# Kernel optimization log

Hardware: AMD Instinct MI355X
Metric: run time of the kernel (lower is better)

The kernel has to match this reference:

```python
import jax, jax.numpy as jnp
import numpy as np

N = 50000
E = 600000
D_IN = 128
D_HID = 128


def gcn_conv(x, src, dst, ew, W, b):
    """PyG-style GCNConv with self-loops and symmetric normalization.
    x: [N, Fin], src/dst: [E'], ew: [E'], W: [Fin, Fout], b: [Fout].
    """
    n = x.shape[0]
    # degree from incoming edge weights (self-loops already appended)
    deg = jax.ops.segment_sum(ew, dst, num_segments=n)
    dinv = jnp.where(deg > 0, jax.lax.rsqrt(deg), 0.0)
    norm = dinv[src] * ew * dinv[dst]  # [E']
    h = x @ W  # linear transform first (PyG order)
    msg = h[src] * norm[:, None]  # gather + scale, [E', Fout]
    out = jax.ops.segment_sum(msg, dst, num_segments=n)  # scatter-add
    return out + b


def setup_inputs() -> dict:
    key = jax.random.key(0)
    k1, k2, k3, k4, k5, k6, k7 = jax.random.split(key, 7)
    x = jax.random.normal(k1, (N, D_IN), dtype=jnp.float32)
    edge_index = jax.random.randint(k2, (2, E), 0, N, dtype=jnp.int64)
    edge_weight = jax.random.uniform(k3, (E,), dtype=jnp.float32)
    s1 = 1.0 / np.sqrt(D_IN)
    s2 = 1.0 / np.sqrt(D_HID)
    W1 = jax.random.uniform(k4, (D_IN, D_HID), dtype=jnp.float32, minval=-s1, maxval=s1)
    b1 = jax.random.uniform(k5, (D_HID,), dtype=jnp.float32, minval=-s1, maxval=s1)
    W2 = jax.random.uniform(k6, (D_HID, D_IN), dtype=jnp.float32, minval=-s2, maxval=s2)
    b2 = jax.random.uniform(k7, (D_IN,), dtype=jnp.float32, minval=-s2, maxval=s2)
    return {"x": x, "edge_index": edge_index, "edge_weight": edge_weight,
            "W1": W1, "b1": b1, "W2": W2, "b2": b2}


def reference(x, edge_index, edge_weight, W1, b1, W2, b2):
    n = x.shape[0]
    loops = jnp.arange(n, dtype=edge_index.dtype)
    src = jnp.concatenate([edge_index[0], loops])
    dst = jnp.concatenate([edge_index[1], loops])
    ew = jnp.concatenate([edge_weight, jnp.ones((n,), dtype=edge_weight.dtype)])
    h = gcn_conv(x, src, dst, ew, W1, b1)
    h = jax.nn.relu(h)
    h = gcn_conv(h, src, dst, ew, W2, b2)
    return jax.nn.sigmoid(h)
```

## Files before the change

kernel.cpp:

```cpp
#include <hip/hip_runtime.h>
#include <math.h>


typedef unsigned int uint32;
typedef unsigned long long u64;
typedef __attribute__((ext_vector_type(8))) short bf16x8;
typedef __attribute__((ext_vector_type(4))) float f32x4;
typedef __attribute__((ext_vector_type(2))) float f32x2;

__device__ __forceinline__ unsigned short f2bf(float f) {
    uint32 b = __float_as_uint(f);
    return (unsigned short)((b + 0x7FFFu + ((b >> 16) & 1u)) >> 16);
}

template <int AFP32, int OUTFP8>
__device__ __forceinline__ void gemm_body(const void* __restrict__ Ap,
                                          const unsigned short* __restrict__ WT,
                                          void* __restrict__ H,
                                          int n, int tb) {
    const int lane = threadIdx.x & 63;
    const int wv   = threadIdx.x >> 6;
    const int quad = lane >> 4;
    const int l16  = lane & 15;
    const int m0   = tb * 128 + wv * 32;
    f32x4 acc[2][8] = {};

    #pragma unroll
    for (int ks = 0; ks < 4; ++ks) {
        const int k0 = ks * 32 + quad * 8;
        bf16x8 a[2];
        #pragma unroll
        for (int rt = 0; rt < 2; ++rt) {
            int row = m0 + rt * 16 + l16;
            if (row >= n) row = n - 1;
            if (AFP32) {
                const float* Af = (const float*)Ap + (size_t)row * 128 + k0;
                float4 f0 = *(const float4*)(Af);
                float4 f1 = *(const float4*)(Af + 4);
                bf16x8 v;
                v[0] = (short)f2bf(f0.x); v[1] = (short)f2bf(f0.y);
                v[2] = (short)f2bf(f0.z); v[3] = (short)f2bf(f0.w);
                v[4] = (short)f2bf(f1.x); v[5] = (short)f2bf(f1.y);
                v[6] = (short)f2bf(f1.z); v[7] = (short)f2bf(f1.w);
                a[rt] = v;
            } else {
                const unsigned short* Ab = (const unsigned short*)Ap + (size_t)row * 128 + k0;
                a[rt] = *(const bf16x8*)Ab;
            }
        }
        #pragma unroll
        for (int ct = 0; ct < 8; ++ct) {
            bf16x8 b = *(const bf16x8*)(WT + (size_t)(ct * 16 + l16) * 128 + k0);
            acc[0][ct] = __builtin_amdgcn_mfma_f32_16x16x32_bf16(a[0], b, acc[0][ct], 0, 0, 0);
            acc[1][ct] = __builtin_amdgcn_mfma_f32_16x16x32_bf16(a[1], b, acc[1][ct], 0, 0, 0);
        }
    }

    #pragma unroll
    for (int rt = 0; rt < 2; ++rt) {
        #pragma unroll
        for (int r = 0; r < 4; ++r) {
            int row = m0 + rt * 16 + quad * 4 + r;
            if (row < n) {
                if (OUTFP8) {
                    unsigned char* o = (unsigned char*)H + (size_t)row * 128 + l16;
                    #pragma unroll
                    for (int cp = 0; cp < 4; ++cp) {
                        int pk = __builtin_amdgcn_cvt_pk_fp8_f32(
                            acc[rt][2 * cp][r], acc[rt][2 * cp + 1][r], 0, false);
                        o[(2 * cp) * 16]     = (unsigned char)(pk & 0xFF);
                        o[(2 * cp + 1) * 16] = (unsigned char)((pk >> 8) & 0xFF);
                    }
                } else {
                    unsigned short* o = (unsigned short*)H + (size_t)row * 128 + l16;
                    #pragma unroll
                    for (int ct = 0; ct < 8; ++ct)
                        o[ct * 16] = f2bf(acc[rt][ct][r]);
                }
            }
        }
    }
}

__global__ __launch_bounds__(256) void k_init(u64* __restrict__ packed, int n4,
                                              int* __restrict__ done,
                                              const float* __restrict__ W1,
                                              const float* __restrict__ W2,
                                              unsigned short* __restrict__ WT1,
                                              unsigned short* __restrict__ WT2) {
    int idx = blockIdx.x * 256 + threadIdx.x;
    if (idx < n4) ((uint4*)packed)[idx] = make_uint4(0u, 0u, 0u, 0u);
    if (idx == 0) *done = 0;
    if (blockIdx.x < 64) {
        int j = blockIdx.x * 256 + threadIdx.x;
        int k = j >> 7, nn = j & 127;
        WT1[nn * 128 + k] = f2bf(W1[k * 128 + nn]);
        WT2[nn * 128 + k] = f2bf(W2[k * 128 + nn]);
    }
}

__global__ __launch_bounds__(256) void k_gemm1_hist(const float* __restrict__ x,
                                                    const unsigned short* __restrict__ WT1,
                                                    unsigned char* __restrict__ h8,
                                                    const int* __restrict__ dst,
                                                    const float* __restrict__ ew,
                                                    u64* __restrict__ packed,
                                                    int* __restrict__ rank,
                                                    int E, int N, int gGemm) {
    const int b = blockIdx.x;
    if (b < gGemm) {
        gemm_body<1, 1>(x, WT1, h8, N, b);
        return;
    }
    int i = (b - gGemm) * 256 + threadIdx.x;
    if (i < E) {
        int d = dst[i];
        int r = (i >> 8) & 7;
        u64 add = (1ULL << 44) + (u64)(ew[i] * 4294967296.0f);
        u64 old = atomicAdd(&packed[(size_t)r * N + d], add);
        rank[i] = (int)(old >> 44);
    }
}

__global__ __launch_bounds__(256) void k_scan(const u64* __restrict__ packed,
                                              float* __restrict__ dinv,
                                              u64* __restrict__ bases,
                                              int* __restrict__ rowptr,
                                              int* __restrict__ csums,
                                              int* __restrict__ done, int nNodes) {
    __shared__ int s[256];
    __shared__ int lastFlag;
    const int t = threadIdx.x;
    const int base = blockIdx.x * 1024 + t * 4;
    const int n = nNodes + 1;
    int v[4];
    #pragma unroll
    for (int u = 0; u < 4; ++u) {
        int idx = base + u;
        int c = 0;
        if (idx < nNodes) {
            const u64 mask = (1ULL << 44) - 1;
            u64 ssum = 0;
            u64 bs = 0;
            uint32 cum = 0;
            #pragma unroll
            for (int r = 0; r < 8; ++r) {
                u64 pv = packed[(size_t)r * nNodes + idx];
                bs |= (u64)cum << (8 * r);
                cum += (uint32)(pv >> 44);
                ssum += (pv & mask);
            }
            c = (int)cum;
            float deg = 1.0f + (float)ssum * (1.0f / 4294967296.0f);
            dinv[idx] = rsqrtf(deg);
            bases[idx] = bs;
        }
        v[u] = c;
    }
    s[t] = v[0] + v[1] + v[2] + v[3];
    __syncthreads();
    #pragma unroll
    for (int off = 1; off < 256; off <<= 1) {
        int x = (t >= off) ? s[t - off] : 0;
        __syncthreads();
        s[t] += x;
        __syncthreads();
    }
    if (t == 255)
        __hip_atomic_store(&csums[blockIdx.x], s[255], __ATOMIC_RELEASE,
                           __HIP_MEMORY_SCOPE_AGENT);
    int e = (t == 0) ? 0 : s[t - 1];
    if (base + 0 < n) rowptr[base + 0] = e;
    if (base + 1 < n) rowptr[base + 1] = e + v[0];
    if (base + 2 < n) rowptr[base + 2] = e + v[0] + v[1];
    if (base + 3 < n) rowptr[base + 3] = e + v[0] + v[1] + v[2];

    __syncthreads();
    if (t == 0) {
        int prev = __hip_atomic_fetch_add(done, 1, __ATOMIC_ACQ_REL,
                                          __HIP_MEMORY_SCOPE_AGENT);
        lastFlag = (prev == (int)gridDim.x - 1);
    }
    __syncthreads();
    if (lastFlag && t < 64) {
        int g = (int)gridDim.x;
        int orig = (t < g) ? __hip_atomic_load(&csums[t], __ATOMIC_ACQUIRE,
                                               __HIP_MEMORY_SCOPE_AGENT)
                           : 0;
        int vv = orig;
        #pragma unroll
        for (int off = 1; off < 64; off <<= 1) {
            int y = __shfl_up(vv, off, 64);
            if (t >= off) vv += y;
        }
        if (t < g) csums[t] = vv - orig;
    }
}

__global__ __launch_bounds__(256) void k_fill(const int* __restrict__ src,
                                              const int* __restrict__ dst,
                                              const float* __restrict__ ew,
                                              const float* __restrict__ dinv,
                                              const int* __restrict__ rowptr,
                                              const int* __restrict__ csums,
                                              const u64* __restrict__ bases,
                                              const int* __restrict__ rank,
                                              float2* __restrict__ csr, int e) {
    int i = blockIdx.x * 256 + threadIdx.x;
    if (i < e) {
        int s = src[i], d = dst[i];
        int r = (i >> 8) & 7;
        float nrm = dinv[s] * ew[i] * dinv[d];
        int pos = rowptr[d] + csums[d >> 10]
                + (int)((bases[d] >> (8 * r)) & 0xFF) + rank[i];
        csr[pos] = make_float2(__int_as_float(s), nrm);
    }
}

__device__ __forceinline__ void fma8_f8(float* acc, uint2 u, float w) {
    f32x2 f;
    f = __builtin_amdgcn_cvt_pk_f32_fp8((int)u.x, false);
    acc[0] += f[0] * w; acc[1] += f[1] * w;
    f = __builtin_amdgcn_cvt_pk_f32_fp8((int)u.x, true);
    acc[2] += f[0] * w; acc[3] += f[1] * w;
    f = __builtin_amdgcn_cvt_pk_f32_fp8((int)u.y, false);
    acc[4] += f[0] * w; acc[5] += f[1] * w;
    f = __builtin_amdgcn_cvt_pk_f32_fp8((int)u.y, true);
    acc[6] += f[0] * w; acc[7] += f[1] * w;
}

__global__ __launch_bounds__(256) void k_ag1(const unsigned char* __restrict__ h8,
                                             const float2* __restrict__ csr,
                                             const int* __restrict__ rowptr,
                                             const int* __restrict__ csums,
                                             const float* __restrict__ dinv,
                                             const float4* __restrict__ bias4,
                                             unsigned char* __restrict__ g8, int N) {
    int node = blockIdx.x * 4 + (threadIdx.x >> 6);
    if (node >= N) return;
    const int lane = threadIdx.x & 63;
    const int q = lane >> 4, l = lane & 15;
    const int start = rowptr[node] + csums[node >> 10];
    const int end   = rowptr[node + 1] + csums[(node + 1) >> 10];
    const uint2* H2 = (const uint2*)h8;

    float di = dinv[node];
    float selfw = (q == 0) ? di * di : 0.0f;
    float acc[8] = {};
    fma8_f8(acc, H2[(size_t)node * 16 + l], selfw);

    for (int k = start; k < end; k += 16) {
        float2 c[4];
        float w[4];
        #pragma unroll
        for (int j = 0; j < 4; ++j) {
            int ej = k + q + 4 * j;
            c[j] = csr[ej < end ? ej : end - 1];
            w[j] = (ej < end) ? c[j].y : 0.0f;
        }
        uint2 u[4];
        #pragma unroll
        for (int j = 0; j < 4; ++j)
            u[j] = H2[(size_t)__float_as_int(c[j].x) * 16 + l];
        #pragma unroll
        for (int j = 0; j < 4; ++j) fma8_f8(acc, u[j], w[j]);
    }

    #pragma unroll
    for (int j = 0; j < 8; ++j) {
        acc[j] += __shfl_xor(acc[j], 16, 64);
        acc[j] += __shfl_xor(acc[j], 32, 64);
    }

    if (q == 0) {
        float4 b0 = bias4[l * 2], b1v = bias4[l * 2 + 1];
        acc[0] += b0.x;  acc[1] += b0.y;  acc[2] += b0.z;  acc[3] += b0.w;
        acc[4] += b1v.x; acc[5] += b1v.y; acc[6] += b1v.z; acc[7] += b1v.w;
        #pragma unroll
        for (int j = 0; j < 8; ++j) acc[j] = fmaxf(acc[j], 0.0f);
        uint2 o;
        int w0 = __builtin_amdgcn_cvt_pk_fp8_f32(acc[0], acc[1], 0, false);
        w0     = __builtin_amdgcn_cvt_pk_fp8_f32(acc[2], acc[3], w0, true);
        int w1 = __builtin_amdgcn_cvt_pk_fp8_f32(acc[4], acc[5], 0, false);
        w1     = __builtin_amdgcn_cvt_pk_fp8_f32(acc[6], acc[7], w1, true);
        o.x = (uint32)w0; o.y = (uint32)w1;
        ((uint2*)g8)[(size_t)node * 16 + l] = o;
    }
}

__global__ __launch_bounds__(256) void k_ag2s(const unsigned char* __restrict__ g8,
                                              const float2* __restrict__ csr,
                                              const int* __restrict__ rowptr,
                                              const int* __restrict__ csums,
                                              const float* __restrict__ dinv,
                                              const float* __restrict__ b2,
                                              const unsigned short* __restrict__ WT2,
                                              float* __restrict__ out, int N) {
    __shared__ unsigned short sA[16][136];
    const int lane = threadIdx.x & 63;
    const int wv   = threadIdx.x >> 6;
    const int q    = lane >> 4;
    const int l    = lane & 15;
    const int nb   = blockIdx.x * 16;
    const uint2* G2 = (const uint2*)g8;

    for (int j = 0; j < 4; ++j) {
        const int node = nb + wv * 4 + j;
        float acc[8] = {};
        if (node < N) {
            const int start = rowptr[node] + csums[node >> 10];
            const int end   = rowptr[node + 1] + csums[(node + 1) >> 10];
            float di = dinv[node];
            float selfw = (q == 0) ? di * di : 0.0f;
            fma8_f8(acc, G2[(size_t)node * 16 + l], selfw);

            for (int k = start; k < end; k += 16) {
                float2 c[4];
                float w[4];
                #pragma unroll
                for (int jj = 0; jj < 4; ++jj) {
                    int ej = k + q + 4 * jj;
                    c[jj] = csr[ej < end ? ej : end - 1];
                    w[jj] = (ej < end) ? c[jj].y : 0.0f;
                }
                uint2 u[4];
                #pragma unroll
                for (int jj = 0; jj < 4; ++jj)
                    u[jj] = G2[(size_t)__float_as_int(c[jj].x) * 16 + l];
                #pragma unroll
                for (int jj = 0; jj < 4; ++jj) fma8_f8(acc, u[jj], w[jj]);
            }
            #pragma unroll
            for (int t = 0; t < 8; ++t) {
                acc[t] += __shfl_xor(acc[t], 16, 64);
                acc[t] += __shfl_xor(acc[t], 32, 64);
            }
        }
        if (q == 0) {
            uint4 o = make_uint4(0u, 0u, 0u, 0u);
            if (node < N) {
                o.x = (uint32)f2bf(acc[0]) | ((uint32)f2bf(acc[1]) << 16);
                o.y = (uint32)f2bf(acc[2]) | ((uint32)f2bf(acc[3]) << 16);
                o.z = (uint32)f2bf(acc[4]) | ((uint32)f2bf(acc[5]) << 16);
                o.w = (uint32)f2bf(acc[6]) | ((uint32)f2bf(acc[7]) << 16);
            }
            *(uint4*)&sA[wv * 4 + j][l * 8] = o;
        }
    }

    __syncthreads();

    f32x4 a2[2] = {};
    #pragma unroll
    for (int ks = 0; ks < 4; ++ks) {
        const int k0 = ks * 32 + q * 8;
        bf16x8 a = *(const bf16x8*)&sA[l][k0];
        #pragma unroll
        for (int ct = 0; ct < 2; ++ct) {
            bf16x8 b = *(const bf16x8*)(WT2 + (size_t)(wv * 32 + ct * 16 + l) * 128 + k0);
            a2[ct] = __builtin_amdgcn_mfma_f32_16x16x32_bf16(a, b, a2[ct], 0, 0, 0);
        }
    }
    #pragma unroll
    for (int ct = 0; ct < 2; ++ct) {
        const int col = wv * 32 + ct * 16 + l;
        const float bb = b2[col];
        #pragma unroll
        for (int r = 0; r < 4; ++r) {
            int row = nb + q * 4 + r;
            if (row < N) {
                float v = a2[ct][r] + bb;
                out[(size_t)row * 128 + col] = 1.0f / (1.0f + expf(-v));
            }
        }
    }
}

extern "C" void kernel_launch(void* const* d_in, const int* in_sizes, int n_in,
                              void* d_out, int out_size, void* d_ws, size_t ws_size,
                              hipStream_t stream) {
    const float* x  = (const float*)d_in[0];
    const int*   ei = (const int*)d_in[1];
    const float* ew = (const float*)d_in[2];
    const float* W1 = (const float*)d_in[3];
    const float* b1 = (const float*)d_in[4];
    const float* W2 = (const float*)d_in[5];
    const float* b2 = (const float*)d_in[6];

    const int N = in_sizes[0] / 128;
    const int E = in_sizes[2];
    const int* src = ei;
    const int* dst = ei + E;
    float* out = (float*)d_out;

    auto align = [](size_t v) { return (v + 255) & ~(size_t)255; };
    char* p = (char*)d_ws;
    float*  dinv   = (float*)p;   p += align((size_t)N * 4);
    int*    rowptr = (int*)p;     p += align((size_t)(N + 1) * 4);
    int*    csums  = (int*)p;     p += align((size_t)1024 * 4);
    int*    done   = (int*)p;     p += align((size_t)256);
    u64*    bases  = (u64*)p;     p += align((size_t)N * 8);
    unsigned short* WT1 = (unsigned short*)p; p += align((size_t)128 * 128 * 2);
    unsigned short* WT2 = (unsigned short*)p; p += align((size_t)128 * 128 * 2);
    int*    rank   = (int*)p;     p += align((size_t)E * 4);
    float2* csr    = (float2*)p;  p += align((size_t)E * 8);
    unsigned char*  h8 = (unsigned char*)p;  p += align((size_t)N * 128);
    unsigned char*  g8 = (unsigned char*)p;
    u64* packed = (u64*)g8;

    const int nbE = (E + 255) / 256;
    const int gScan = (N + 1 + 1023) / 1024;
    const int gGemm = (N + 127) / 128;
    const int gAg1  = (N + 3) / 4;
    const int gAg2  = (N + 15) / 16;
    const int n4 = N * 4;
    const int gInit = ((n4 + 255) / 256) < 64 ? 64 : ((n4 + 255) / 256);

    k_init<<<gInit, 256, 0, stream>>>(packed, n4, done, W1, W2, WT1, WT2);
    k_gemm1_hist<<<gGemm + nbE, 256, 0, stream>>>(x, WT1, h8, dst, ew, packed,
                                                  rank, E, N, gGemm);
    k_scan<<<gScan, 256, 0, stream>>>(packed, dinv, bases, rowptr, csums, done, N);
    k_fill<<<nbE, 256, 0, stream>>>(src, dst, ew, dinv, rowptr, csums, bases,
                                    rank, csr, E);

    k_ag1<<<gAg1, 256, 0, stream>>>(h8, csr, rowptr, csums, dinv,
                                    (const float4*)b1, g8, N);

    k_ag2s<<<gAg2, 256, 0, stream>>>(g8, csr, rowptr, csums, dinv, b2,
                                     WT2, out, N);
}
```

Baseline: 201.5 us.

## Map one node per 16-lane quarter-wave in both aggregation kernels

Both SpMM aggregation kernels now give each 16-lane group its own destination node, where before a whole wave shared one node and split its edges across four quarters. Each group walks its node's edges eight at a time with deeper unrolled gathers, so the cross-quarter shuffle reduction is gone and more independent loads are in flight. The k_ag1 grid shrinks to match. In exchange, nodes of different degree within one wave diverge, and each node's edge loop runs serially within its group.

```diff
diff --git a/kernel.cpp b/kernel.cpp
--- a/kernel.cpp
+++ b/kernel.cpp
@@ -229,6 +229,27 @@
     acc[6] += f[0] * w; acc[7] += f[1] * w;
 }
 
+__device__ __forceinline__ void gather_q8(float* acc, const uint2* __restrict__ T,
+                                          const float2* __restrict__ csr,
+                                          int start, int end, int l) {
+    for (int k = start; k < end; k += 8) {
+        float2 c[8];
+        float w[8];
+        uint2 u[8];
+        #pragma unroll
+        for (int j = 0; j < 8; ++j) {
+            int ej = k + j;
+            c[j] = csr[ej < end ? ej : end - 1];
+            w[j] = (ej < end) ? c[j].y : 0.0f;
+        }
+        #pragma unroll
+        for (int j = 0; j < 8; ++j)
+            u[j] = T[(size_t)__float_as_int(c[j].x) * 16 + l];
+        #pragma unroll
+        for (int j = 0; j < 8; ++j) fma8_f8(acc, u[j], w[j]);
+    }
+}
+
 __global__ __launch_bounds__(256) void k_ag1(const unsigned char* __restrict__ h8,
                                              const float2* __restrict__ csr,
                                              const int* __restrict__ rowptr,
@@ -236,56 +257,31 @@
                                              const float* __restrict__ dinv,
                                              const float4* __restrict__ bias4,
                                              unsigned char* __restrict__ g8, int N) {
-    int node = blockIdx.x * 4 + (threadIdx.x >> 6);
-    if (node >= N) return;
     const int lane = threadIdx.x & 63;
     const int q = lane >> 4, l = lane & 15;
+    const int node = blockIdx.x * 16 + (threadIdx.x >> 6) * 4 + q;
+    if (node >= N) return;
+    const uint2* H2 = (const uint2*)h8;
     const int start = rowptr[node] + csums[node >> 10];
     const int end   = rowptr[node + 1] + csums[(node + 1) >> 10];
-    const uint2* H2 = (const uint2*)h8;
-
-    float di = dinv[node];
-    float selfw = (q == 0) ? di * di : 0.0f;
+    const float di = dinv[node];
+
     float acc[8] = {};
-    fma8_f8(acc, H2[(size_t)node * 16 + l], selfw);
-
-    for (int k = start; k < end; k += 16) {
-        float2 c[4];
-        float w[4];
-        #pragma unroll
-        for (int j = 0; j < 4; ++j) {
-            int ej = k + q + 4 * j;
-            c[j] = csr[ej < end ? ej : end - 1];
-            w[j] = (ej < end) ? c[j].y : 0.0f;
-        }
-        uint2 u[4];
-        #pragma unroll
-        for (int j = 0; j < 4; ++j)
-            u[j] = H2[(size_t)__float_as_int(c[j].x) * 16 + l];
-        #pragma unroll
-        for (int j = 0; j < 4; ++j) fma8_f8(acc, u[j], w[j]);
-    }
-
-    #pragma unroll
-    for (int j = 0; j < 8; ++j) {
-        acc[j] += __shfl_xor(acc[j], 16, 64);
-        acc[j] += __shfl_xor(acc[j], 32, 64);
-    }
-
-    if (q == 0) {
-        float4 b0 = bias4[l * 2], b1v = bias4[l * 2 + 1];
-        acc[0] += b0.x;  acc[1] += b0.y;  acc[2] += b0.z;  acc[3] += b0.w;
-        acc[4] += b1v.x; acc[5] += b1v.y; acc[6] += b1v.z; acc[7] += b1v.w;
-        #pragma unroll
-        for (int j = 0; j < 8; ++j) acc[j] = fmaxf(acc[j], 0.0f);
-        uint2 o;
-        int w0 = __builtin_amdgcn_cvt_pk_fp8_f32(acc[0], acc[1], 0, false);
-        w0     = __builtin_amdgcn_cvt_pk_fp8_f32(acc[2], acc[3], w0, true);
-        int w1 = __builtin_amdgcn_cvt_pk_fp8_f32(acc[4], acc[5], 0, false);
-        w1     = __builtin_amdgcn_cvt_pk_fp8_f32(acc[6], acc[7], w1, true);
-        o.x = (uint32)w0; o.y = (uint32)w1;
-        ((uint2*)g8)[(size_t)node * 16 + l] = o;
-    }
+    fma8_f8(acc, H2[(size_t)node * 16 + l], di * di);
+    gather_q8(acc, H2, csr, start, end, l);
+
+    float4 b0 = bias4[l * 2], b1v = bias4[l * 2 + 1];
+    acc[0] += b0.x;  acc[1] += b0.y;  acc[2] += b0.z;  acc[3] += b0.w;
+    acc[4] += b1v.x; acc[5] += b1v.y; acc[6] += b1v.z; acc[7] += b1v.w;
+    #pragma unroll
+    for (int j = 0; j < 8; ++j) acc[j] = fmaxf(acc[j], 0.0f);
+    uint2 o;
+    int w0 = __builtin_amdgcn_cvt_pk_fp8_f32(acc[0], acc[1], 0, false);
+    w0     = __builtin_amdgcn_cvt_pk_fp8_f32(acc[2], acc[3], w0, true);
+    int w1 = __builtin_amdgcn_cvt_pk_fp8_f32(acc[4], acc[5], 0, false);
+    w1     = __builtin_amdgcn_cvt_pk_fp8_f32(acc[6], acc[7], w1, true);
+    o.x = (uint32)w0; o.y = (uint32)w1;
+    ((uint2*)g8)[(size_t)node * 16 + l] = o;
 }
 
 __global__ __launch_bounds__(256) void k_ag2s(const unsigned char* __restrict__ g8,
@@ -302,51 +298,25 @@
     const int q    = lane >> 4;
     const int l    = lane & 15;
     const int nb   = blockIdx.x * 16;
+    const int node = nb + wv * 4 + q;
     const uint2* G2 = (const uint2*)g8;
 
-    for (int j = 0; j < 4; ++j) {
-        const int node = nb + wv * 4 + j;
-        float acc[8] = {};
-        if (node < N) {
-            const int start = rowptr[node] + csums[node >> 10];
-            const int end   = rowptr[node + 1] + csums[(node + 1) >> 10];
-            float di = dinv[node];
-            float selfw = (q == 0) ? di * di : 0.0f;
-            fma8_f8(acc, G2[(size_t)node * 16 + l], selfw);
-
-            for (int k = start; k < end; k += 16) {
-                float2 c[4];
-                float w[4];
-                #pragma unroll
-                for (int jj = 0; jj < 4; ++jj) {
-                    int ej = k + q + 4 * jj;
-                    c[jj] = csr[ej < end ? ej : end - 1];
-                    w[jj] = (ej < end) ? c[jj].y : 0.0f;
-                }
-                uint2 u[4];
-                #pragma unroll
-                for (int jj = 0; jj < 4; ++jj)
-                    u[jj] = G2[(size_t)__float_as_int(c[jj].x) * 16 + l];
-                #pragma unroll
-                for (int jj = 0; jj < 4; ++jj) fma8_f8(acc, u[jj], w[jj]);
-            }
-            #pragma unroll
-            for (int t = 0; t < 8; ++t) {
-                acc[t] += __shfl_xor(acc[t], 16, 64);
-                acc[t] += __shfl_xor(acc[t], 32, 64);
-            }
-        }
-        if (q == 0) {
-            uint4 o = make_uint4(0u, 0u, 0u, 0u);
-            if (node < N) {
-                o.x = (uint32)f2bf(acc[0]) | ((uint32)f2bf(acc[1]) << 16);
-                o.y = (uint32)f2bf(acc[2]) | ((uint32)f2bf(acc[3]) << 16);
-                o.z = (uint32)f2bf(acc[4]) | ((uint32)f2bf(acc[5]) << 16);
-                o.w = (uint32)f2bf(acc[6]) | ((uint32)f2bf(acc[7]) << 16);
-            }
-            *(uint4*)&sA[wv * 4 + j][l * 8] = o;
-        }
-    }
+    float acc[8] = {};
+    if (node < N) {
+        const int start = rowptr[node] + csums[node >> 10];
+        const int end   = rowptr[node + 1] + csums[(node + 1) >> 10];
+        const float di = dinv[node];
+        fma8_f8(acc, G2[(size_t)node * 16 + l], di * di);
+        gather_q8(acc, G2, csr, start, end, l);
+    }
+    uint4 o = make_uint4(0u, 0u, 0u, 0u);
+    if (node < N) {
+        o.x = (uint32)f2bf(acc[0]) | ((uint32)f2bf(acc[1]) << 16);
+        o.y = (uint32)f2bf(acc[2]) | ((uint32)f2bf(acc[3]) << 16);
+        o.z = (uint32)f2bf(acc[4]) | ((uint32)f2bf(acc[5]) << 16);
+        o.w = (uint32)f2bf(acc[6]) | ((uint32)f2bf(acc[7]) << 16);
+    }
+    *(uint4*)&sA[wv * 4 + q][l * 8] = o;
 
     __syncthreads();
 
@@ -411,7 +381,7 @@
     const int nbE = (E + 255) / 256;
     const int gScan = (N + 1 + 1023) / 1024;
     const int gGemm = (N + 127) / 128;
-    const int gAg1  = (N + 3) / 4;
+    const int gAg1  = (N + 15) / 16;
     const int gAg2  = (N + 15) / 16;
     const int n4 = N * 4;
     const int gInit = ((n4 + 255) / 256) < 64 ? 64 : ((n4 + 255) / 256);
```

Result: faster. 190.2 us (-5.6%).
